# Performance work log

Hardware: AMD Instinct MI355X
Metric: run time of the kernel (lower is better)

## Reference

```python
import jax, jax.numpy as jnp
import numpy as np

N_NODES = 50000
N_EDGES = 800000
D = 128


def setup_inputs() -> dict:
    key = jax.random.key(0)
    ks = jax.random.split(key, 5)
    x = jax.random.normal(ks[0], (N_NODES, D), dtype=jnp.float32)
    edge_index = jax.random.randint(ks[1], (2, N_EDGES), 0, N_NODES, dtype=jnp.int64)
    # GCNConv linear weight + bias, and the two DGCN parameters
    Wc = jax.random.normal(ks[2], (D, D), dtype=jnp.float32) / np.sqrt(D)
    bc = jnp.zeros((D,), dtype=jnp.float32)
    W0 = jax.random.normal(ks[3], (D, D), dtype=jnp.float32)
    Wt = jax.random.normal(ks[4], (D, D), dtype=jnp.float32)
    return {"x": x, "edge_index": edge_index, "Wc": Wc, "bc": bc, "W0": W0, "Wt": Wt}


def gcn_conv(x, edge_index, Wc, bc):
    # PyG GCNConv: add self-loops, symmetric normalization D^-1/2 (A+I) D^-1/2,
    # applied to x @ Wc, plus bias.
    n = x.shape[0]
    loops = jnp.arange(n, dtype=edge_index.dtype)
    src = jnp.concatenate([edge_index[0], loops])  # [E+N]
    dst = jnp.concatenate([edge_index[1], loops])
    ones = jnp.ones(src.shape[0], dtype=x.dtype)
    deg = jax.ops.segment_sum(ones, dst, num_segments=n)  # in-degree incl. self-loop
    dinv = jnp.where(deg > 0, jax.lax.rsqrt(deg), 0.0)
    norm = dinv[src] * dinv[dst]  # [E+N]
    xw = x @ Wc  # [N, D]
    msgs = xw[src] * norm[:, None]  # gather + scale  [E+N, D]
    agg = jax.ops.segment_sum(msgs, dst, num_segments=n)  # scatter-add  [N, D]
    return agg + bc


def reference(x, edge_index, Wc, bc, W0, Wt):
    h_neigh = gcn_conv(x, edge_index, Wc, bc)
    h_self = x @ W0
    h_change = (h_neigh - x) @ Wt
    return h_neigh + h_self + h_change
```

## Files before the change

kernel.cpp:

```cpp
#include <hip/hip_runtime.h>

#define N_NODES 50000
#define N_EDGES 800000
#define D 128
#define NB 391
#define CAPB 4928
#define P1B 256
#define EPB ((N_EDGES + P1B - 1) / P1B)
#define CAP 16
#define WPB 16
#define XC0 (P1B + WPB + 1)
#define KA_BLOCKS (XC0 + (N_NODES * 16) / 256)

typedef __attribute__((ext_vector_type(8))) short short8;
typedef __attribute__((ext_vector_type(4))) float f32x4;

__device__ __forceinline__ unsigned short f2bf(float f) {
    unsigned int u = __builtin_bit_cast(unsigned int, f);
    u += 0x7FFFu + ((u >> 16) & 1u);
    return (unsigned short)(u >> 16);
}
__device__ __forceinline__ float bf2f(unsigned short h) {
    unsigned int u = ((unsigned int)h) << 16;
    return __builtin_bit_cast(float, u);
}

__global__ void k_init(int* __restrict__ gcur) {
    const int t = threadIdx.x;
    if (t < NB) gcur[t] = 0;
}

__global__ __launch_bounds__(256) void k_a(const int* __restrict__ src,
                                           const int* __restrict__ dst,
                                           int* __restrict__ gcur,
                                           unsigned int* __restrict__ pbuf,
                                           const float* __restrict__ Wc,
                                           const float* __restrict__ W0,
                                           const float* __restrict__ Wt,
                                           const float* __restrict__ bc,
                                           const float* __restrict__ x,
                                           unsigned short* __restrict__ Wp,
                                           float* __restrict__ bv,
                                           unsigned short* __restrict__ xb) {
    __shared__ unsigned int stage[NB][CAP + 1];
    __shared__ int scnt[NB];
    const int t = threadIdx.x;
    const unsigned int bid = blockIdx.x;

    if (bid < P1B) {
        for (int i = t; i < NB; i += 256) scnt[i] = 0;
        __syncthreads();

        const long e0 = (long)bid * EPB;
        const long e1 = (e0 + EPB < N_EDGES) ? e0 + EPB : N_EDGES;
        for (long e = e0 + t; e < e1; e += 256) {
            const int s = src[e];
            const int d = dst[e];
            const int b = d >> 7;
            const unsigned int p = ((unsigned int)(d & 127) << 16) | (unsigned int)s;
            const int slot = atomicAdd(&scnt[b], 1);
            if (slot < CAP) {
                stage[b][slot] = p;
            } else {
                pbuf[(long)b * CAPB + atomicAdd(&gcur[b], 1)] = p;
            }
        }
        __syncthreads();
        for (int bb = t; bb < NB; bb += 256) {
            const int n = (scnt[bb] < CAP) ? scnt[bb] : CAP;
            if (n > 0) {
                const int pos = bb * CAPB + atomicAdd(&gcur[bb], n);
                for (int i = 0; i < n; ++i) pbuf[pos + i] = stage[bb][i];
            }
        }
        return;
    }

    if (bid < P1B + WPB) {
        const int id = (int)(bid - P1B) * 256 + t;
        const int lane = id & 63;
        const int tile = (id >> 6) & 7;
        const int step = id >> 9;
        const int n = tile * 16 + (lane & 15);
        const int kbase = step * 32 + (lane >> 4) * 8;
        float f[8];
#pragma unroll
        for (int j = 0; j < 8; ++j) {
            const int k = kbase + j;
            f[j] = (k < D) ? Wc[k * D + n]
                           : (W0[(k - D) * D + n] - Wt[(k - D) * D + n]);
        }
        if (kbase < D) {
#pragma unroll 8
            for (int m = 0; m < D; ++m) {
                const float wt = Wt[m * D + n];
#pragma unroll
                for (int j = 0; j < 8; ++j) f[j] += Wc[(kbase + j) * D + m] * wt;
            }
        }
        unsigned short v[8];
#pragma unroll
        for (int j = 0; j < 8; ++j) v[j] = f2bf(f[j]);
        *(uint4*)(Wp + (long)id * 8) = *(uint4*)v;
        return;
    }

    if (bid == P1B + WPB) {
        if (t < D) {
            float acc = bc[t];
#pragma unroll 16
            for (int k = 0; k < D; ++k) acc += bc[k] * Wt[k * D + t];
            bv[t] = acc;
        }
        return;
    }

    const int gid = (int)(bid - XC0) * 256 + t;
    const int node = gid >> 4;
    const int c = gid & 15;
    const float4 a = ((const float4*)x)[(long)node * 32 + c * 2];
    const float4 b = ((const float4*)x)[(long)node * 32 + c * 2 + 1];
    const float f[8] = {a.x, a.y, a.z, a.w, b.x, b.y, b.z, b.w};
    unsigned short vb[8];
#pragma unroll
    for (int j = 0; j < 8; ++j) vb[j] = f2bf(f[j]);
    *(uint4*)(xb + (long)node * 128 + c * 8) = *(uint4*)vb;
}

__global__ __launch_bounds__(256) void k_part2(const unsigned int* __restrict__ pbuf,
                                               const int* __restrict__ gcur,
                                               int* __restrict__ row_start,
                                               int* __restrict__ cnt,
                                               float* __restrict__ dinv,
                                               int* __restrict__ esrc) {
    __shared__ int lcnt[128];
    __shared__ int lcur[128];
    __shared__ int stmp[128];
    const int b = blockIdx.x;
    const int t = threadIdx.x;
    const int base = b * CAPB;
    const int n = gcur[b];

    if (t < 128) lcnt[t] = 0;
    __syncthreads();
    for (int i = t; i < n; i += 256) atomicAdd(&lcnt[pbuf[base + i] >> 16], 1);
    __syncthreads();

    int c = 0;
    if (t < 128) {
        c = lcnt[t];
        stmp[t] = c;
    }
    __syncthreads();
    for (int off = 1; off < 128; off <<= 1) {
        int u = (t >= off && t < 128) ? stmp[t - off] : 0;
        __syncthreads();
        if (t < 128) stmp[t] += u;
        __syncthreads();
    }
    if (t < 128) {
        const int ls = base + stmp[t] - c;
        lcur[t] = ls;
        const int node = b * 128 + t;
        if (node < N_NODES) {
            row_start[node] = ls;
            cnt[node] = c;
            dinv[node] = rsqrtf((float)c + 1.0f);
        }
    }
    __syncthreads();

    for (int i = t; i < n; i += 256) {
        const unsigned int p = pbuf[base + i];
        const int pos = atomicAdd(&lcur[p >> 16], 1);
        esrc[pos] = (int)(p & 0xFFFFu);
    }
}

__global__ __launch_bounds__(512) void k_gmm(const unsigned short* __restrict__ xb,
                                             const int* __restrict__ row_start,
                                             const int* __restrict__ cnt,
                                             const float* __restrict__ dinv,
                                             const int* __restrict__ esrc,
                                             const unsigned short* __restrict__ Wp,
                                             const float* __restrict__ bv,
                                             float* __restrict__ out) {
    __shared__ unsigned short sg[64 * 128];
    const int tid = threadIdx.x;
    const int wave = tid >> 6;
    const int lane = tid & 63;
    const int c = lane & 15;
    const int s = lane >> 4;
    const int row0 = blockIdx.x * 64;

    int beg[8], en[8];
#pragma unroll
    for (int m = 0; m < 8; ++m) {
        const int node = row0 + wave * 8 + m;
        const bool v = node < N_NODES;
        const int b0 = v ? row_start[node] : 0;
        beg[m] = b0;
        en[m] = b0 + (v ? cnt[node] : 0);
    }

#pragma unroll
    for (int m = 0; m < 8; ++m) {
        const int node = row0 + wave * 8 + m;
        const bool valid = node < N_NODES;
        float acc[8] = {};
        int i = beg[m] + s;
        const int end = en[m];
        for (; i + 12 < end; i += 16) {
            const int a0 = esrc[i];
            const int a1 = esrc[i + 4];
            const int a2 = esrc[i + 8];
            const int a3 = esrc[i + 12];
            const short8 v0 = *(const short8*)(xb + (long)a0 * 128 + c * 8);
            const short8 v1 = *(const short8*)(xb + (long)a1 * 128 + c * 8);
            const short8 v2 = *(const short8*)(xb + (long)a2 * 128 + c * 8);
            const short8 v3 = *(const short8*)(xb + (long)a3 * 128 + c * 8);
            const float d0 = dinv[a0];
            const float d1 = dinv[a1];
            const float d2 = dinv[a2];
            const float d3 = dinv[a3];
#pragma unroll
            for (int j = 0; j < 8; ++j)
                acc[j] += (d0 * bf2f((unsigned short)v0[j]) +
                           d1 * bf2f((unsigned short)v1[j])) +
                          (d2 * bf2f((unsigned short)v2[j]) +
                           d3 * bf2f((unsigned short)v3[j]));
        }
        for (; i < end; i += 4) {
            const int a0 = esrc[i];
            const float d0 = dinv[a0];
            const short8 v0 = *(const short8*)(xb + (long)a0 * 128 + c * 8);
#pragma unroll
            for (int j = 0; j < 8; ++j) acc[j] += d0 * bf2f((unsigned short)v0[j]);
        }
#pragma unroll
        for (int j = 0; j < 8; ++j) {
            acc[j] += __shfl_xor(acc[j], 16);
            acc[j] += __shfl_xor(acc[j], 32);
        }
        if (s == 0) {
            const int r = wave * 8 + m;
            unsigned short o[8] = {0, 0, 0, 0, 0, 0, 0, 0};
            if (valid) {
                const float di = dinv[node];
                const short8 xs = *(const short8*)(xb + (long)node * 128 + c * 8);
#pragma unroll
                for (int j = 0; j < 8; ++j)
                    o[j] = f2bf(di * (acc[j] + di * bf2f((unsigned short)xs[j])));
            }
            const int col = (c * 16) ^ ((r & 7) << 4);
            *(uint4*)((char*)sg + r * 256 + col) = *(uint4*)o;
        }
    }
    __syncthreads();

    const int lr = lane & 15;
    const int quad = lane >> 4;
    const int wr = wave & 3;
    const int wc = wave >> 2;
    const int rloc = wr * 16 + lr;
    int ar = row0 + rloc;
    if (ar >= N_NODES) ar = N_NODES - 1;
    const unsigned short* aptr = xb + (long)ar * 128 + quad * 8;

    f32x4 acc2[4] = {};
#pragma unroll
    for (int s8 = 0; s8 < 8; ++s8) {
        short8 a;
        if (s8 < 4) {
            const int colb = (s8 * 64 + quad * 16) ^ ((rloc & 7) << 4);
            a = *(const short8*)((const char*)sg + rloc * 256 + colb);
        } else {
            a = *(const short8*)(aptr + (s8 - 4) * 32);
        }
#pragma unroll
        for (int t2 = 0; t2 < 4; ++t2) {
            const short8 b =
                *(const short8*)(Wp + ((long)(s8 * 8 + wc * 4 + t2) * 64 + lane) * 8);
            acc2[t2] = __builtin_amdgcn_mfma_f32_16x16x32_bf16(a, b, acc2[t2], 0, 0, 0);
        }
    }

    const int rowbase = row0 + wr * 16;
#pragma unroll
    for (int t2 = 0; t2 < 4; ++t2) {
        const int col = wc * 64 + t2 * 16 + lr;
        const float bvv = bv[col];
#pragma unroll
        for (int r = 0; r < 4; ++r) {
            const int row = rowbase + quad * 4 + r;
            if (row < N_NODES) out[(long)row * D + col] = acc2[t2][r] + bvv;
        }
    }
}

extern "C" void kernel_launch(void* const* d_in, const int* in_sizes, int n_in,
                              void* d_out, int out_size, void* d_ws, size_t ws_size,
                              hipStream_t stream) {
    const float* x  = (const float*)d_in[0];
    const int*   ei = (const int*)d_in[1];
    const float* Wc = (const float*)d_in[2];
    const float* bc = (const float*)d_in[3];
    const float* W0 = (const float*)d_in[4];
    const float* Wt = (const float*)d_in[5];
    float* out = (float*)d_out;

    const int* src = ei;
    const int* dst = ei + N_EDGES;

    unsigned short* xb = (unsigned short*)d_ws;
    int*   cnt        = (int*)(xb + (size_t)N_NODES * 128);
    int*   row_start  = cnt + N_NODES;
    float* dinv       = (float*)(row_start + N_NODES);
    int*   esrc       = (int*)(dinv + N_NODES);
    unsigned int* pbuf = (unsigned int*)(esrc + (size_t)NB * CAPB);
    float* bv         = (float*)(pbuf + (size_t)NB * CAPB);
    unsigned short* Wp = (unsigned short*)(bv + D);
    int*   gcur       = (int*)(Wp + 256 * D);

    k_init<<<1, 512, 0, stream>>>(gcur);
    k_a<<<KA_BLOCKS, 256, 0, stream>>>(src, dst, gcur, pbuf, Wc, W0, Wt, bc, x,
                                       Wp, bv, xb);
    k_part2<<<NB, 256, 0, stream>>>(pbuf, gcur, row_start, cnt, dinv, esrc);
    k_gmm<<<(N_NODES + 63) / 64, 512, 0, stream>>>(xb, row_start, cnt, dinv, esrc,
                                                   Wp, bv, out);
}
```

Measured before the change: 176.2 us.

## Sort neighbours by source quarter and interleave eight node gathers per wave

The partition kernel now buckets each destination's edges into four sub-buckets by the high bits of the source index. It stores four 8-bit counts per node in a packed word. The gather kernel processes all eight of a wave's nodes together, one source-quarter at a time. This is meant to give more independent loads in flight and better L2 locality on the bf16 feature table. The cost is padding work to the maximum count among the eight nodes, a larger histogram and scan, counts that silently saturate at 255 per quarter, and bounds guards on the partition buffer.

```diff
diff --git a/kernel.cpp b/kernel.cpp
--- a/kernel.cpp
+++ b/kernel.cpp
@@ -62,15 +62,17 @@
             if (slot < CAP) {
                 stage[b][slot] = p;
             } else {
-                pbuf[(long)b * CAPB + atomicAdd(&gcur[b], 1)] = p;
+                const int pos = atomicAdd(&gcur[b], 1);
+                if (pos < CAPB) pbuf[(long)b * CAPB + pos] = p;
             }
         }
         __syncthreads();
         for (int bb = t; bb < NB; bb += 256) {
             const int n = (scnt[bb] < CAP) ? scnt[bb] : CAP;
             if (n > 0) {
-                const int pos = bb * CAPB + atomicAdd(&gcur[bb], n);
-                for (int i = 0; i < n; ++i) pbuf[pos + i] = stage[bb][i];
+                const int pos = atomicAdd(&gcur[bb], n);
+                for (int i = 0; i < n; ++i)
+                    if (pos + i < CAPB) pbuf[(long)bb * CAPB + pos + i] = stage[bb][i];
             }
         }
         return;
@@ -130,56 +132,71 @@
 __global__ __launch_bounds__(256) void k_part2(const unsigned int* __restrict__ pbuf,
                                                const int* __restrict__ gcur,
                                                int* __restrict__ row_start,
-                                               int* __restrict__ cnt,
+                                               unsigned int* __restrict__ cnt4,
                                                float* __restrict__ dinv,
                                                int* __restrict__ esrc) {
-    __shared__ int lcnt[128];
-    __shared__ int lcur[128];
-    __shared__ int stmp[128];
+    __shared__ int h[512];
+    __shared__ int ps[256];
+    __shared__ int lcur[512];
     const int b = blockIdx.x;
     const int t = threadIdx.x;
-    const int base = b * CAPB;
-    const int n = gcur[b];
-
-    if (t < 128) lcnt[t] = 0;
-    __syncthreads();
-    for (int i = t; i < n; i += 256) atomicAdd(&lcnt[pbuf[base + i] >> 16], 1);
-    __syncthreads();
-
-    int c = 0;
+    const long base = (long)b * CAPB;
+    int n = gcur[b];
+    if (n > CAPB) n = CAPB;
+
+    h[t] = 0;
+    h[t + 256] = 0;
+    __syncthreads();
+    for (int i = t; i < n; i += 256) {
+        const unsigned int p = pbuf[base + i];
+        const int key = (int)((p >> 16) << 2) | (int)((p & 0xFFFFu) >> 14);
+        atomicAdd(&h[key], 1);
+    }
+    __syncthreads();
+
+    const int a0 = h[2 * t];
+    const int a1 = h[2 * t + 1];
+    ps[t] = a0 + a1;
+    __syncthreads();
+    for (int off = 1; off < 256; off <<= 1) {
+        const int u = (t >= off) ? ps[t - off] : 0;
+        __syncthreads();
+        ps[t] += u;
+        __syncthreads();
+    }
+    const int ep = ps[t] - a0 - a1;
+    lcur[2 * t] = (int)base + ep;
+    lcur[2 * t + 1] = (int)base + ep + a0;
+    __syncthreads();
+
     if (t < 128) {
-        c = lcnt[t];
-        stmp[t] = c;
-    }
-    __syncthreads();
-    for (int off = 1; off < 128; off <<= 1) {
-        int u = (t >= off && t < 128) ? stmp[t - off] : 0;
-        __syncthreads();
-        if (t < 128) stmp[t] += u;
-        __syncthreads();
-    }
-    if (t < 128) {
-        const int ls = base + stmp[t] - c;
-        lcur[t] = ls;
         const int node = b * 128 + t;
         if (node < N_NODES) {
-            row_start[node] = ls;
-            cnt[node] = c;
-            dinv[node] = rsqrtf((float)c + 1.0f);
+            row_start[node] = lcur[4 * t];
+            int c0 = h[4 * t], c1 = h[4 * t + 1], c2 = h[4 * t + 2], c3 = h[4 * t + 3];
+            const int dg = c0 + c1 + c2 + c3;
+            c0 = c0 > 255 ? 255 : c0;
+            c1 = c1 > 255 ? 255 : c1;
+            c2 = c2 > 255 ? 255 : c2;
+            c3 = c3 > 255 ? 255 : c3;
+            cnt4[node] = (unsigned)c0 | ((unsigned)c1 << 8) | ((unsigned)c2 << 16) |
+                         ((unsigned)c3 << 24);
+            dinv[node] = rsqrtf((float)dg + 1.0f);
         }
     }
     __syncthreads();
 
     for (int i = t; i < n; i += 256) {
         const unsigned int p = pbuf[base + i];
-        const int pos = atomicAdd(&lcur[p >> 16], 1);
+        const int key = (int)((p >> 16) << 2) | (int)((p & 0xFFFFu) >> 14);
+        const int pos = atomicAdd(&lcur[key], 1);
         esrc[pos] = (int)(p & 0xFFFFu);
     }
 }
 
 __global__ __launch_bounds__(512) void k_gmm(const unsigned short* __restrict__ xb,
                                              const int* __restrict__ row_start,
-                                             const int* __restrict__ cnt,
+                                             const unsigned int* __restrict__ cnt4,
                                              const float* __restrict__ dinv,
                                              const int* __restrict__ esrc,
                                              const unsigned short* __restrict__ Wp,
@@ -193,64 +210,75 @@
     const int s = lane >> 4;
     const int row0 = blockIdx.x * 64;
 
-    int beg[8], en[8];
+    int cur[8];
+    unsigned int cc[8];
+    float acc[8][8];
 #pragma unroll
     for (int m = 0; m < 8; ++m) {
         const int node = row0 + wave * 8 + m;
         const bool v = node < N_NODES;
-        const int b0 = v ? row_start[node] : 0;
-        beg[m] = b0;
-        en[m] = b0 + (v ? cnt[node] : 0);
+        cur[m] = v ? row_start[node] : 0;
+        cc[m] = v ? cnt4[node] : 0u;
+#pragma unroll
+        for (int j = 0; j < 8; ++j) acc[m][j] = 0.0f;
+    }
+
+#pragma unroll
+    for (int r = 0; r < 4; ++r) {
+        int cN[8];
+        int mxc = 0;
+#pragma unroll
+        for (int m = 0; m < 8; ++m) {
+            cN[m] = (int)((cc[m] >> (8 * r)) & 255u);
+            mxc = (cN[m] > mxc) ? cN[m] : mxc;
+        }
+        for (int k0 = 0; k0 < mxc; k0 += 4) {
+            const int kk = k0 + s;
+            int a[8];
+            float w[8];
+#pragma unroll
+            for (int m = 0; m < 8; ++m) {
+                const bool ok = kk < cN[m];
+                a[m] = ok ? esrc[cur[m] + kk] : 0;
+                w[m] = ok ? 1.0f : 0.0f;
+            }
+            float d[8];
+#pragma unroll
+            for (int m = 0; m < 8; ++m) d[m] = w[m] * dinv[a[m]];
+            short8 v[8];
+#pragma unroll
+            for (int m = 0; m < 8; ++m)
+                v[m] = *(const short8*)(xb + (long)a[m] * 128 + c * 8);
+#pragma unroll
+            for (int m = 0; m < 8; ++m)
+#pragma unroll
+                for (int j = 0; j < 8; ++j)
+                    acc[m][j] += d[m] * bf2f((unsigned short)v[m][j]);
+        }
+#pragma unroll
+        for (int m = 0; m < 8; ++m) cur[m] += cN[m];
     }
 
 #pragma unroll
     for (int m = 0; m < 8; ++m) {
-        const int node = row0 + wave * 8 + m;
-        const bool valid = node < N_NODES;
-        float acc[8] = {};
-        int i = beg[m] + s;
-        const int end = en[m];
-        for (; i + 12 < end; i += 16) {
-            const int a0 = esrc[i];
-            const int a1 = esrc[i + 4];
-            const int a2 = esrc[i + 8];
-            const int a3 = esrc[i + 12];
-            const short8 v0 = *(const short8*)(xb + (long)a0 * 128 + c * 8);
-            const short8 v1 = *(const short8*)(xb + (long)a1 * 128 + c * 8);
-            const short8 v2 = *(const short8*)(xb + (long)a2 * 128 + c * 8);
-            const short8 v3 = *(const short8*)(xb + (long)a3 * 128 + c * 8);
-            const float d0 = dinv[a0];
-            const float d1 = dinv[a1];
-            const float d2 = dinv[a2];
-            const float d3 = dinv[a3];
-#pragma unroll
-            for (int j = 0; j < 8; ++j)
-                acc[j] += (d0 * bf2f((unsigned short)v0[j]) +
-                           d1 * bf2f((unsigned short)v1[j])) +
-                          (d2 * bf2f((unsigned short)v2[j]) +
-                           d3 * bf2f((unsigned short)v3[j]));
-        }
-        for (; i < end; i += 4) {
-            const int a0 = esrc[i];
-            const float d0 = dinv[a0];
-            const short8 v0 = *(const short8*)(xb + (long)a0 * 128 + c * 8);
-#pragma unroll
-            for (int j = 0; j < 8; ++j) acc[j] += d0 * bf2f((unsigned short)v0[j]);
-        }
+        float t8[8];
 #pragma unroll
         for (int j = 0; j < 8; ++j) {
-            acc[j] += __shfl_xor(acc[j], 16);
-            acc[j] += __shfl_xor(acc[j], 32);
+            float v = acc[m][j];
+            v += __shfl_xor(v, 16);
+            v += __shfl_xor(v, 32);
+            t8[j] = v;
         }
         if (s == 0) {
             const int r = wave * 8 + m;
+            const int node = row0 + r;
             unsigned short o[8] = {0, 0, 0, 0, 0, 0, 0, 0};
-            if (valid) {
+            if (node < N_NODES) {
                 const float di = dinv[node];
                 const short8 xs = *(const short8*)(xb + (long)node * 128 + c * 8);
 #pragma unroll
                 for (int j = 0; j < 8; ++j)
-                    o[j] = f2bf(di * (acc[j] + di * bf2f((unsigned short)xs[j])));
+                    o[j] = f2bf(di * (t8[j] + di * bf2f((unsigned short)xs[j])));
             }
             const int col = (c * 16) ^ ((r & 7) << 4);
             *(uint4*)((char*)sg + r * 256 + col) = *(uint4*)o;
@@ -270,18 +298,19 @@
     f32x4 acc2[4] = {};
 #pragma unroll
     for (int s8 = 0; s8 < 8; ++s8) {
-        short8 a;
+        short8 afrag;
         if (s8 < 4) {
             const int colb = (s8 * 64 + quad * 16) ^ ((rloc & 7) << 4);
-            a = *(const short8*)((const char*)sg + rloc * 256 + colb);
+            afrag = *(const short8*)((const char*)sg + rloc * 256 + colb);
         } else {
-            a = *(const short8*)(aptr + (s8 - 4) * 32);
+            afrag = *(const short8*)(aptr + (s8 - 4) * 32);
         }
 #pragma unroll
         for (int t2 = 0; t2 < 4; ++t2) {
-            const short8 b =
+            const short8 bfrag =
                 *(const short8*)(Wp + ((long)(s8 * 8 + wc * 4 + t2) * 64 + lane) * 8);
-            acc2[t2] = __builtin_amdgcn_mfma_f32_16x16x32_bf16(a, b, acc2[t2], 0, 0, 0);
+            acc2[t2] =
+                __builtin_amdgcn_mfma_f32_16x16x32_bf16(afrag, bfrag, acc2[t2], 0, 0, 0);
         }
     }
 
@@ -312,20 +341,20 @@
     const int* src = ei;
     const int* dst = ei + N_EDGES;
 
-    unsigned short* xb = (unsigned short*)d_ws;
-    int*   cnt        = (int*)(xb + (size_t)N_NODES * 128);
-    int*   row_start  = cnt + N_NODES;
-    float* dinv       = (float*)(row_start + N_NODES);
-    int*   esrc       = (int*)(dinv + N_NODES);
-    unsigned int* pbuf = (unsigned int*)(esrc + (size_t)NB * CAPB);
-    float* bv         = (float*)(pbuf + (size_t)NB * CAPB);
-    unsigned short* Wp = (unsigned short*)(bv + D);
-    int*   gcur       = (int*)(Wp + 256 * D);
+    unsigned short* xb  = (unsigned short*)d_ws;
+    int* row_start      = (int*)(xb + (size_t)N_NODES * 128);
+    unsigned int* cnt4  = (unsigned int*)(row_start + N_NODES);
+    float* dinv         = (float*)(cnt4 + N_NODES);
+    int* esrc           = (int*)(dinv + N_NODES);
+    unsigned int* pbuf  = (unsigned int*)(esrc + (size_t)NB * CAPB);
+    float* bv           = (float*)(pbuf + (size_t)NB * CAPB);
+    unsigned short* Wp  = (unsigned short*)(bv + D);
+    int* gcur           = (int*)(Wp + 256 * D);
 
     k_init<<<1, 512, 0, stream>>>(gcur);
     k_a<<<KA_BLOCKS, 256, 0, stream>>>(src, dst, gcur, pbuf, Wc, W0, Wt, bc, x,
                                        Wp, bv, xb);
-    k_part2<<<NB, 256, 0, stream>>>(pbuf, gcur, row_start, cnt, dinv, esrc);
-    k_gmm<<<(N_NODES + 63) / 64, 512, 0, stream>>>(xb, row_start, cnt, dinv, esrc,
+    k_part2<<<NB, 256, 0, stream>>>(pbuf, gcur, row_start, cnt4, dinv, esrc);
+    k_gmm<<<(N_NODES + 63) / 64, 512, 0, stream>>>(xb, row_start, cnt4, dinv, esrc,
                                                    Wp, bv, out);
 }
```

Result: slower. 219.7 us (+24.7%).
